# Optimization experiments

Measured on AMD Instinct MI355X. Metric: run time of the kernel, lower is better.

Reference implementation:

```python
import jax, jax.numpy as jnp
import numpy as np

NUM_NODES = 200000
NODE_DIM = 256
MSG_DIM = 2 * NODE_DIM + 1 + 172  # 685
NUM_UPDATES = 65536


def setup_inputs() -> dict:
    key = jax.random.key(0)
    ks = jax.random.split(key, 7)
    H3 = 3 * NODE_DIM
    return {
        "memory": jax.random.normal(ks[0], (NUM_NODES, NODE_DIM), jnp.float32),
        "messages": jax.random.normal(ks[1], (NUM_UPDATES, MSG_DIM), jnp.float32),
        "node_idx": jax.random.randint(ks[2], (NUM_UPDATES,), 0, NUM_NODES, jnp.int64 if jax.config.jax_enable_x64 else jnp.int32),
        "W_ih": jax.random.normal(ks[3], (H3, MSG_DIM), jnp.float32) * 0.05,
        "W_hh": jax.random.normal(ks[4], (H3, NODE_DIM), jnp.float32) * 0.05,
        "b_ih": jax.random.normal(ks[5], (H3,), jnp.float32) * 0.05,
        "b_hh": jax.random.normal(ks[6], (H3,), jnp.float32) * 0.05,
    }


def reference(memory, messages, node_idx, W_ih, W_hh, b_ih, b_hh):
    # Batched equivalent of: for each (node, msg): mem[node] = GRUCell(msg, mem[node])
    h = memory[node_idx]                                   # [U, H] gather
    gi = messages @ W_ih.T + b_ih                          # [U, 3H]
    gh = h @ W_hh.T + b_hh                                 # [U, 3H]
    i_r, i_z, i_n = jnp.split(gi, 3, axis=-1)
    h_r, h_z, h_n = jnp.split(gh, 3, axis=-1)
    r = jax.nn.sigmoid(i_r + h_r)
    z = jax.nn.sigmoid(i_z + h_z)
    n = jnp.tanh(i_n + r * h_n)
    h_new = (1.0 - z) * n + z * h                          # torch GRUCell update
    return memory.at[node_idx].set(h_new)                  # scatter back into memory
```

## Files before the change

### kernel.cpp

```cpp
#include <hip/hip_runtime.h>
#include <cstdint>
#include <cstddef>

#define NUM_NODES 200000
#define NODE_DIM  256
#define MSG_DIM   685
#define NUM_UPD   65536
#define KPAD      960
#define NOUT      1024

typedef __bf16 bf16;
typedef bf16  bf16x8 __attribute__((ext_vector_type(8)));
typedef float f32x4  __attribute__((ext_vector_type(4)));

__device__ inline void async_load16(const void* g, void* l) {
    __builtin_amdgcn_global_load_lds(
        (const __attribute__((address_space(1))) void*)g,
        (__attribute__((address_space(3))) void*)l,
        16, 0, 0);
}

__device__ inline float sigmoidf_(float x) { return 1.0f / (1.0f + __expf(-x)); }
__device__ inline float tanhf_(float x)    { return 1.0f - 2.0f / (1.0f + __expf(2.0f * x)); }

__global__ void k_winner(const int* __restrict__ idx, int* __restrict__ winner) {
    int u = blockIdx.x * 256 + threadIdx.x;
    atomicMax(&winner[idx[u]], u);
}

__global__ void k_copy(const float* __restrict__ mem, const int* __restrict__ winner,
                       float* __restrict__ out) {
    int row = blockIdx.x * 4 + (threadIdx.x >> 6);
    int c   = threadIdx.x & 63;
    if (winner[row] >= 0) return;
    const float4* src = (const float4*)(mem + (size_t)row * NODE_DIM);
    float4*       dst = (float4*)(out + (size_t)row * NODE_DIM);
    dst[c] = src[c];
}

__global__ void k_prep_wc(const float* __restrict__ W_ih, const float* __restrict__ W_hh,
                          bf16* __restrict__ Wc) {
    int n = blockIdx.x;
    int ntile = n >> 4, cc = n & 15;
    int gate = ntile & 3;
    int dim  = (ntile >> 2) * 16 + cc;
    for (int i = 0; i < 4; i++) {
        int k = i * 256 + (int)threadIdx.x;
        if (k >= KPAD) break;
        float v = 0.f;
        if (k < MSG_DIM) {
            if (gate == 0)      v = W_ih[(size_t)dim * MSG_DIM + k];
            else if (gate == 1) v = W_ih[(size_t)(256 + dim) * MSG_DIM + k];
            else if (gate == 2) v = W_ih[(size_t)(512 + dim) * MSG_DIM + k];
        } else if (k < MSG_DIM + NODE_DIM) {
            int j = k - MSG_DIM;
            if (gate == 0)      v = W_hh[(size_t)dim * NODE_DIM + j];
            else if (gate == 1) v = W_hh[(size_t)(256 + dim) * NODE_DIM + j];
            else if (gate == 3) v = W_hh[(size_t)(512 + dim) * NODE_DIM + j];
        }
        Wc[(size_t)n * KPAD + k] = (bf16)v;
    }
}

__global__ void k_prep_x(const float* __restrict__ msgs, const float* __restrict__ mem,
                         const int* __restrict__ idx, bf16* __restrict__ X) {
    int u = blockIdx.x;
    int node = idx[u];
    const float* mrow = msgs + (size_t)u * MSG_DIM;
    const float* hrow = mem + (size_t)node * NODE_DIM;
    bf16* xrow = X + (size_t)u * KPAD;
    for (int k = threadIdx.x; k < KPAD; k += 256) {
        float v = 0.f;
        if (k < MSG_DIM)                  v = mrow[k];
        else if (k < MSG_DIM + NODE_DIM)  v = hrow[k - MSG_DIM];
        xrow[k] = (bf16)v;
    }
}

__global__ __launch_bounds__(256) void k_gemm(
        const bf16* __restrict__ X, const bf16* __restrict__ Wc,
        const float* __restrict__ mem, const int* __restrict__ idx,
        const int* __restrict__ winner,
        const float* __restrict__ b_ih, const float* __restrict__ b_hh,
        float* __restrict__ out) {
    __shared__ bf16 As[128 * 64];
    __shared__ bf16 Bs[128 * 64];

    const int tid = threadIdx.x;
    const int w = tid >> 6, l = tid & 63;
    const int wr = w >> 1, wc = w & 1;
    const int quad = l >> 4, c = l & 15;

    const int bn = blockIdx.x & 7;
    const int bm = blockIdx.x >> 3;

    f32x4 acc[4][4];
    #pragma unroll
    for (int i = 0; i < 4; i++)
        #pragma unroll
        for (int j = 0; j < 4; j++) acc[i][j] = (f32x4){0.f, 0.f, 0.f, 0.f};

    const int flatr = (tid * 8) >> 6;
    const int flatc = (tid * 8) & 63;
    const bf16* gA = X  + (size_t)(bm * 128) * KPAD;
    const bf16* gB = Wc + (size_t)(bn * 128) * KPAD;

    for (int kt = 0; kt < KPAD / 64; kt++) {
        const int k0 = kt * 64;
        #pragma unroll
        for (int j = 0; j < 4; j++) {
            int r = j * 32 + flatr;
            async_load16(gA + (size_t)r * KPAD + k0 + flatc, (void*)(As + j * 2048 + w * 512));
        }
        #pragma unroll
        for (int j = 0; j < 4; j++) {
            int r = j * 32 + flatr;
            async_load16(gB + (size_t)r * KPAD + k0 + flatc, (void*)(Bs + j * 2048 + w * 512));
        }
        __syncthreads();
        #pragma unroll
        for (int kk = 0; kk < 2; kk++) {
            bf16x8 a[4], b[4];
            #pragma unroll
            for (int mi = 0; mi < 4; mi++)
                a[mi] = *(const bf16x8*)&As[(wr * 64 + mi * 16 + c) * 64 + kk * 32 + quad * 8];
            #pragma unroll
            for (int ni = 0; ni < 4; ni++)
                b[ni] = *(const bf16x8*)&Bs[(wc * 64 + ni * 16 + c) * 64 + kk * 32 + quad * 8];
            #pragma unroll
            for (int mi = 0; mi < 4; mi++)
                #pragma unroll
                for (int ni = 0; ni < 4; ni++)
                    acc[mi][ni] = __builtin_amdgcn_mfma_f32_16x16x32_bf16(a[mi], b[ni], acc[mi][ni], 0, 0, 0);
        }
        __syncthreads();
    }

    const int dim = (bn * 2 + wc) * 16 + c;
    const float br  = b_ih[dim]       + b_hh[dim];
    const float bz  = b_ih[256 + dim] + b_hh[256 + dim];
    const float bin = b_ih[512 + dim];
    const float bhn = b_hh[512 + dim];

    #pragma unroll
    for (int mi = 0; mi < 4; mi++) {
        #pragma unroll
        for (int v = 0; v < 4; v++) {
            int u = bm * 128 + wr * 64 + mi * 16 + quad * 4 + v;
            int node = idx[u];
            if (winner[node] != u) continue;
            float r  = sigmoidf_(acc[mi][0][v] + br);
            float z  = sigmoidf_(acc[mi][1][v] + bz);
            float nn = tanhf_(acc[mi][2][v] + bin + r * (acc[mi][3][v] + bhn));
            float h  = mem[(size_t)node * NODE_DIM + dim];
            out[(size_t)node * NODE_DIM + dim] = (1.f - z) * nn + z * h;
        }
    }
}

extern "C" void kernel_launch(void* const* d_in, const int* in_sizes, int n_in,
                              void* d_out, int out_size, void* d_ws, size_t ws_size,
                              hipStream_t stream) {
    const float* memory   = (const float*)d_in[0];
    const float* messages = (const float*)d_in[1];
    const int*   node_idx = (const int*)d_in[2];
    const float* W_ih     = (const float*)d_in[3];
    const float* W_hh     = (const float*)d_in[4];
    const float* b_ih     = (const float*)d_in[5];
    const float* b_hh     = (const float*)d_in[6];
    float* out = (float*)d_out;

    char* ws = (char*)d_ws;
    bf16* X  = (bf16*)ws;
    bf16* Wc = (bf16*)(ws + (size_t)NUM_UPD * KPAD * 2);
    int* winner = (int*)(ws + (size_t)NUM_UPD * KPAD * 2 + (size_t)NOUT * KPAD * 2);

    hipMemsetAsync(winner, 0xFF, NUM_NODES * sizeof(int), stream);
    k_winner <<<NUM_UPD / 256, 256, 0, stream>>>(node_idx, winner);
    k_copy   <<<NUM_NODES / 4, 256, 0, stream>>>(memory, winner, out);
    k_prep_wc<<<NOUT, 256, 0, stream>>>(W_ih, W_hh, Wc);
    k_prep_x <<<NUM_UPD, 256, 0, stream>>>(messages, memory, node_idx, X);
    k_gemm   <<<(NUM_UPD / 128) * (NOUT / 128), 256, 0, stream>>>(
        X, Wc, memory, node_idx, winner, b_ih, b_hh, out);
}
```

Measured before the change: 818.9 us.

## Rework GEMM to 256x256 double-buffered swizzled tiles and vectorize prep kernels

The GEMM moves to 256x256 tiles with 512 threads, double-buffered LDS, XOR-swizzled layout, manual ds_read_b128 with explicit waitcnt/barrier scheduling, setprio around MFMA, and a block remap for L2 locality. The prep_x kernel now does vectorized bf16 packing with an aligned hidden-state offset (688), and k_copy becomes a grid-stride loop. These changes target load latency, LDS bank conflicts and per-element overhead, at the cost of more registers and fragile hand-written synchronization.

```diff
diff --git a/kernel.cpp b/kernel.cpp
--- a/kernel.cpp
+++ b/kernel.cpp
@@ -7,21 +7,44 @@
 #define MSG_DIM   685
 #define NUM_UPD   65536
 #define KPAD      960
+#define H_OFF     688
+#define H_END     944
 #define NOUT      1024
+#define NT        (KPAD / 64)
 
 typedef __bf16 bf16;
 typedef bf16  bf16x8 __attribute__((ext_vector_type(8)));
 typedef float f32x4  __attribute__((ext_vector_type(4)));
-
-__device__ inline void async_load16(const void* g, void* l) {
+typedef int   i32x4  __attribute__((ext_vector_type(4)));
+
+__device__ __forceinline__ void async_load16(const void* g, void* l) {
     __builtin_amdgcn_global_load_lds(
         (const __attribute__((address_space(1))) void*)g,
         (__attribute__((address_space(3))) void*)l,
         16, 0, 0);
 }
 
+__device__ __forceinline__ uint32_t lds_off(const void* p) {
+    return (uint32_t)(uintptr_t)(__attribute__((address_space(3))) const void*)p;
+}
+
+__device__ __forceinline__ bf16x8 dsr128(uint32_t addr) {
+    i32x4 r;
+    asm volatile("ds_read_b128 %0, %1" : "=v"(r) : "v"(addr));
+    return __builtin_bit_cast(bf16x8, r);
+}
+
+__device__ __forceinline__ unsigned short f2bf(float v) {
+    return __builtin_bit_cast(unsigned short, (bf16)v);
+}
+
 __device__ inline float sigmoidf_(float x) { return 1.0f / (1.0f + __expf(-x)); }
 __device__ inline float tanhf_(float x)    { return 1.0f - 2.0f / (1.0f + __expf(2.0f * x)); }
+
+#define BAR  __builtin_amdgcn_s_barrier()
+#define LGKM0 do { asm volatile("s_waitcnt lgkmcnt(0)" ::: "memory"); \
+                   __builtin_amdgcn_sched_barrier(0); } while (0)
+#define VMW(n) asm volatile("s_waitcnt vmcnt(" #n ")" ::: "memory")
 
 __global__ void k_winner(const int* __restrict__ idx, int* __restrict__ winner) {
     int u = blockIdx.x * 256 + threadIdx.x;
@@ -30,12 +53,14 @@
 
 __global__ void k_copy(const float* __restrict__ mem, const int* __restrict__ winner,
                        float* __restrict__ out) {
-    int row = blockIdx.x * 4 + (threadIdx.x >> 6);
-    int c   = threadIdx.x & 63;
-    if (winner[row] >= 0) return;
-    const float4* src = (const float4*)(mem + (size_t)row * NODE_DIM);
-    float4*       dst = (float4*)(out + (size_t)row * NODE_DIM);
-    dst[c] = src[c];
+    int wv = threadIdx.x >> 6;
+    int c  = threadIdx.x & 63;
+    for (int row = blockIdx.x * 4 + wv; row < NUM_NODES; row += 2048 * 4) {
+        if (winner[row] >= 0) continue;
+        const float4* src = (const float4*)(mem + (size_t)row * NODE_DIM);
+        float4*       dst = (float4*)(out + (size_t)row * NODE_DIM);
+        dst[c] = src[c];
+    }
 }
 
 __global__ void k_prep_wc(const float* __restrict__ W_ih, const float* __restrict__ W_hh,
@@ -52,8 +77,8 @@
             if (gate == 0)      v = W_ih[(size_t)dim * MSG_DIM + k];
             else if (gate == 1) v = W_ih[(size_t)(256 + dim) * MSG_DIM + k];
             else if (gate == 2) v = W_ih[(size_t)(512 + dim) * MSG_DIM + k];
-        } else if (k < MSG_DIM + NODE_DIM) {
-            int j = k - MSG_DIM;
+        } else if (k >= H_OFF && k < H_END) {
+            int j = k - H_OFF;
             if (gate == 0)      v = W_hh[(size_t)dim * NODE_DIM + j];
             else if (gate == 1) v = W_hh[(size_t)(256 + dim) * NODE_DIM + j];
             else if (gate == 3) v = W_hh[(size_t)(512 + dim) * NODE_DIM + j];
@@ -65,88 +90,147 @@
 __global__ void k_prep_x(const float* __restrict__ msgs, const float* __restrict__ mem,
                          const int* __restrict__ idx, bf16* __restrict__ X) {
     int u = blockIdx.x;
-    int node = idx[u];
-    const float* mrow = msgs + (size_t)u * MSG_DIM;
-    const float* hrow = mem + (size_t)node * NODE_DIM;
+    int t = threadIdx.x;
     bf16* xrow = X + (size_t)u * KPAD;
-    for (int k = threadIdx.x; k < KPAD; k += 256) {
-        float v = 0.f;
-        if (k < MSG_DIM)                  v = mrow[k];
-        else if (k < MSG_DIM + NODE_DIM)  v = hrow[k - MSG_DIM];
-        xrow[k] = (bf16)v;
-    }
-}
-
-__global__ __launch_bounds__(256) void k_gemm(
+    if (t < 344) {
+        const float* mrow = msgs + (size_t)u * MSG_DIM;
+        int c0 = 2 * t;
+        float v0 = (c0     < MSG_DIM) ? mrow[c0]     : 0.f;
+        float v1 = (c0 + 1 < MSG_DIM) ? mrow[c0 + 1] : 0.f;
+        ushort2 p; p.x = f2bf(v0); p.y = f2bf(v1);
+        ((ushort2*)xrow)[t] = p;
+    } else if (t < 408) {
+        int j = t - 344;
+        const float4* h4p = (const float4*)(mem + (size_t)idx[u] * NODE_DIM);
+        float4 h4 = h4p[j];
+        ushort4 p; p.x = f2bf(h4.x); p.y = f2bf(h4.y); p.z = f2bf(h4.z); p.w = f2bf(h4.w);
+        ((ushort4*)(xrow + H_OFF))[j] = p;
+    } else if (t < 412) {
+        int j = t - 408;
+        ushort4 z; z.x = z.y = z.z = z.w = 0;
+        ((ushort4*)(xrow + H_END))[j] = z;
+    }
+}
+
+__global__ __launch_bounds__(512, 2) void k_gemm(
         const bf16* __restrict__ X, const bf16* __restrict__ Wc,
         const float* __restrict__ mem, const int* __restrict__ idx,
         const int* __restrict__ winner,
         const float* __restrict__ b_ih, const float* __restrict__ b_hh,
         float* __restrict__ out) {
-    __shared__ bf16 As[128 * 64];
-    __shared__ bf16 Bs[128 * 64];
+    __shared__ __align__(128) bf16 lds[2 * 2 * 16384];
 
     const int tid = threadIdx.x;
-    const int w = tid >> 6, l = tid & 63;
-    const int wr = w >> 1, wc = w & 1;
+    const int w  = tid >> 6, l = tid & 63;
+    const int wr = w >> 2,  wc = w & 3;
     const int quad = l >> 4, c = l & 15;
 
-    const int bn = blockIdx.x & 7;
-    const int bm = blockIdx.x >> 3;
-
-    f32x4 acc[4][4];
+    const int bid = blockIdx.x;
+    const int wg  = (bid & 7) * 128 + (bid >> 3);
+    const int bm  = wg >> 2;
+    const int bn  = wg & 3;
+
+    f32x4 acc[8][4];
     #pragma unroll
-    for (int i = 0; i < 4; i++)
+    for (int i = 0; i < 8; i++)
         #pragma unroll
         for (int j = 0; j < 4; j++) acc[i][j] = (f32x4){0.f, 0.f, 0.f, 0.f};
 
-    const int flatr = (tid * 8) >> 6;
-    const int flatc = (tid * 8) & 63;
-    const bf16* gA = X  + (size_t)(bm * 128) * KPAD;
-    const bf16* gB = Wc + (size_t)(bn * 128) * KPAD;
-
-    for (int kt = 0; kt < KPAD / 64; kt++) {
-        const int k0 = kt * 64;
-        #pragma unroll
-        for (int j = 0; j < 4; j++) {
-            int r = j * 32 + flatr;
-            async_load16(gA + (size_t)r * KPAD + k0 + flatc, (void*)(As + j * 2048 + w * 512));
-        }
-        #pragma unroll
-        for (int j = 0; j < 4; j++) {
-            int r = j * 32 + flatr;
-            async_load16(gB + (size_t)r * KPAD + k0 + flatc, (void*)(Bs + j * 2048 + w * 512));
-        }
-        __syncthreads();
-        #pragma unroll
-        for (int kk = 0; kk < 2; kk++) {
-            bf16x8 a[4], b[4];
-            #pragma unroll
-            for (int mi = 0; mi < 4; mi++)
-                a[mi] = *(const bf16x8*)&As[(wr * 64 + mi * 16 + c) * 64 + kk * 32 + quad * 8];
-            #pragma unroll
-            for (int ni = 0; ni < 4; ni++)
-                b[ni] = *(const bf16x8*)&Bs[(wc * 64 + ni * 16 + c) * 64 + kk * 32 + quad * 8];
-            #pragma unroll
-            for (int mi = 0; mi < 4; mi++)
-                #pragma unroll
-                for (int ni = 0; ni < 4; ni++)
-                    acc[mi][ni] = __builtin_amdgcn_mfma_f32_16x16x32_bf16(a[mi], b[ni], acc[mi][ni], 0, 0, 0);
-        }
-        __syncthreads();
-    }
-
-    const int dim = (bn * 2 + wc) * 16 + c;
+    const int srow  = tid >> 3;
+    const int scol8 = (((tid & 7) ^ (srow & 7)) << 3);
+    const bf16* gAt = X  + ((size_t)(bm * 256) + srow) * KPAD + scol8;
+    const bf16* gBt = Wc + ((size_t)(bn * 256) + srow) * KPAD + scol8;
+    const int wofs = w << 9;
+
+    #define STAGE_A(cn) async_load16(gAt + (size_t)(cn) * 64 * KPAD + (size_t)(t + 1) * 64, \
+                                     lds + (nxt << 15) + (cn) * 4096 + wofs)
+    #define STAGE_B(cn) async_load16(gBt + (size_t)(cn) * 64 * KPAD + (size_t)(t + 1) * 64, \
+                                     lds + (nxt << 15) + 16384 + (cn) * 4096 + wofs)
+
+    const uint32_t L0 = lds_off(lds);
+    const uint32_t slot = (uint32_t)((quad ^ (c & 7)) << 4);
+    const uint32_t aA = (uint32_t)(wr * 128 + c) * 128 + slot;
+    const uint32_t aB = 32768u + (uint32_t)(wc * 64 + c) * 128 + slot;
+
+    #define MFMA_HALF(mh) do {                                                   \
+        __builtin_amdgcn_s_setprio(1);                                           \
+        _Pragma("unroll")                                                        \
+        for (int i_ = 0; i_ < 4; i_++) {                                         \
+            _Pragma("unroll")                                                    \
+            for (int j_ = 0; j_ < 4; j_++)                                       \
+                acc[(mh) * 4 + i_][j_] = __builtin_amdgcn_mfma_f32_16x16x32_bf16( \
+                    af[i_], bfr[j_], acc[(mh) * 4 + i_][j_], 0, 0, 0);           \
+        }                                                                        \
+        __builtin_amdgcn_s_setprio(0);                                           \
+    } while (0)
+
+    {
+        #pragma unroll
+        for (int cn = 0; cn < 4; cn++)
+            async_load16(gAt + (size_t)cn * 64 * KPAD, lds + cn * 4096 + wofs);
+        #pragma unroll
+        for (int cn = 0; cn < 4; cn++)
+            async_load16(gBt + (size_t)cn * 64 * KPAD, lds + 16384 + cn * 4096 + wofs);
+        VMW(0);
+        BAR;
+    }
+
+    #pragma unroll 1
+    for (int t = 0; t < NT; ++t) {
+        const int cur = t & 1, nxt = cur ^ 1;
+        const bool stg = (t < NT - 1);
+        const uint32_t bA = L0 + (uint32_t)(cur << 16) + aA;
+        const uint32_t bB = L0 + (uint32_t)(cur << 16) + aB;
+        const uint32_t cA = bA ^ 64u, cB = bB ^ 64u;
+        bf16x8 af[4], bfr[4];
+
+        af[0] = dsr128(bA);          af[1] = dsr128(bA + 2048);
+        af[2] = dsr128(bA + 4096);   af[3] = dsr128(bA + 6144);
+        bfr[0] = dsr128(bB);         bfr[1] = dsr128(bB + 2048);
+        bfr[2] = dsr128(bB + 4096);  bfr[3] = dsr128(bB + 6144);
+        if (stg) { STAGE_B(0); STAGE_B(1); }
+        BAR; LGKM0;
+        MFMA_HALF(0);
+        if (t == NT - 1) { VMW(0); } else { VMW(2); }
+        BAR;
+
+        af[0] = dsr128(bA + 8192);   af[1] = dsr128(bA + 10240);
+        af[2] = dsr128(bA + 12288);  af[3] = dsr128(bA + 14336);
+        if (stg) { STAGE_B(2); STAGE_B(3); }
+        BAR; LGKM0;
+        MFMA_HALF(1);
+        BAR;
+
+        af[0] = dsr128(cA);          af[1] = dsr128(cA + 2048);
+        af[2] = dsr128(cA + 4096);   af[3] = dsr128(cA + 6144);
+        bfr[0] = dsr128(cB);         bfr[1] = dsr128(cB + 2048);
+        bfr[2] = dsr128(cB + 4096);  bfr[3] = dsr128(cB + 6144);
+        if (stg) { STAGE_A(0); STAGE_A(2); }
+        BAR; LGKM0;
+        MFMA_HALF(0);
+        BAR;
+
+        af[0] = dsr128(cA + 8192);   af[1] = dsr128(cA + 10240);
+        af[2] = dsr128(cA + 12288);  af[3] = dsr128(cA + 14336);
+        if (stg) { STAGE_A(1); STAGE_A(3); }
+        BAR; LGKM0;
+        MFMA_HALF(1);
+        VMW(2);
+        BAR;
+    }
+
+    const int dim = (bn * 4 + wc) * 16 + c;
     const float br  = b_ih[dim]       + b_hh[dim];
     const float bz  = b_ih[256 + dim] + b_hh[256 + dim];
     const float bin = b_ih[512 + dim];
     const float bhn = b_hh[512 + dim];
 
     #pragma unroll
-    for (int mi = 0; mi < 4; mi++) {
+    for (int mi = 0; mi < 8; mi++) {
+        const int ubase = bm * 256 + wr * 128 + mi * 16 + quad * 4;
         #pragma unroll
         for (int v = 0; v < 4; v++) {
-            int u = bm * 128 + wr * 64 + mi * 16 + quad * 4 + v;
+            int u = ubase + v;
             int node = idx[u];
             if (winner[node] != u) continue;
             float r  = sigmoidf_(acc[mi][0][v] + br);
@@ -156,6 +240,9 @@
             out[(size_t)node * NODE_DIM + dim] = (1.f - z) * nn + z * h;
         }
     }
+    #undef STAGE_A
+    #undef STAGE_B
+    #undef MFMA_HALF
 }
 
 extern "C" void kernel_launch(void* const* d_in, const int* in_sizes, int n_in,
@@ -177,9 +264,9 @@
 
     hipMemsetAsync(winner, 0xFF, NUM_NODES * sizeof(int), stream);
     k_winner <<<NUM_UPD / 256, 256, 0, stream>>>(node_idx, winner);
-    k_copy   <<<NUM_NODES / 4, 256, 0, stream>>>(memory, winner, out);
+    k_copy   <<<2048, 256, 0, stream>>>(memory, winner, out);
     k_prep_wc<<<NOUT, 256, 0, stream>>>(W_ih, W_hh, Wc);
-    k_prep_x <<<NUM_UPD, 256, 0, stream>>>(messages, memory, node_idx, X);
-    k_gemm   <<<(NUM_UPD / 128) * (NOUT / 128), 256, 0, stream>>>(
+    k_prep_x <<<NUM_UPD, 448, 0, stream>>>(messages, memory, node_idx, X);
+    k_gemm   <<<(NUM_UPD / 256) * (NOUT / 256), 512, 0, stream>>>(
         X, Wc, memory, node_idx, winner, b_ih, b_hh, out);
 }
```

Result: faster. 749.9 us (-8.4%).
